# Optimization experiments

Measured on AMD Instinct MI355X. Metric: run time of the kernel, lower is better.

The kernel has to match this reference:

```python
import jax, jax.numpy as jnp
import numpy as np

WINDOW_LENGTH = 128
PAD = WINDOW_LENGTH // 2  # ReflectionPad1d(window_length/2)


def _hanning(w_len, dtype):
    n = jnp.arange(w_len, dtype=jnp.float32)
    w = 0.5 - 0.5 * jnp.cos(2.0 * jnp.pi * n / (w_len - 1))
    return w.astype(dtype)


def setup_inputs() -> dict:
    key = jax.random.key(0)
    seq = jax.random.normal(key, (16, 512, 64), dtype=jnp.float32)
    return {"seq": seq}


def reference(seq):
    B, L, C = seq.shape
    w = _hanning(WINDOW_LENGTH, seq.dtype)  # [W]
    # reflection pad along time, then strided framing via a gather (replaces the cat loop)
    padded = jnp.pad(seq, ((0, 0), (PAD, PAD), (0, 0)), mode="reflect")  # [B, L+2*PAD, C]
    idx = jnp.arange(L)[:, None] + jnp.arange(WINDOW_LENGTH)[None, :]  # [L, W]
    frames = padded[:, idx, :] * w[None, None, :, None]  # [B, L, W, C]
    cube = jnp.fft.rfft(frames, axis=2)  # [B, L, F=W//2+1, C] complex64
    # complex standardization over dims (1, 2): zero-mean, unit second moment per (batch, channel)
    mu = jnp.mean(cube, axis=(1, 2), keepdims=True)
    centered = cube - mu
    std = jnp.sqrt(jnp.mean(jnp.abs(centered) ** 2, axis=(1, 2), keepdims=True))
    normed = centered / std
    return jnp.abs(normed)  # amplitude of the standardized freq cube, [B, L, F, C]
```

## Files before the change

### kernel.cpp

```cpp
#include <hip/hip_runtime.h>
#include <math.h>


#define B_ 16
#define L_ 512
#define C_ 64
#define W_ 128
#define F_ 65
#define LP 640
#define NLF (L_ * F_)

constexpr double kPI = 3.14159265358979323846;

constexpr double csin_(double x) {
  while (x > kPI) x -= 2.0 * kPI;
  while (x < -kPI) x += 2.0 * kPI;
  double t = x, s = x, x2 = x * x;
  for (int i = 1; i <= 24; ++i) {
    t *= -x2 / ((2.0 * i) * (2.0 * i + 1.0));
    s += t;
  }
  return s;
}
constexpr double ccos_(double x) { return csin_(kPI / 2.0 - x); }

constexpr int bitrev6(int n) {
  int r = 0;
  for (int i = 0; i < 6; ++i) r |= ((n >> i) & 1) << (5 - i);
  return r;
}

struct Tables {
  float win[128];
  float walt[128];
  float w2[128];
  float wg[128];
  float twr[32], twi[32];
  float cur[32], cui[32];
  constexpr Tables() : win(), walt(), w2(), wg(), twr(), twi(), cur(), cui() {
    for (int n = 0; n < 128; ++n) {
      const double wd = 0.5 - 0.5 * ccos_(2.0 * kPI * n / 127.0);
      win[n] = (float)wd;
      walt[n] = (n & 1) ? (float)(-wd) : (float)wd;
      w2[n] = (float)(wd * wd);
      if (n == 0) {
        wg[n] = 0.0f;
      } else {
        const double G = csin_(kPI * n / 2.0) * csin_(65.0 * kPI * n / 128.0) /
                         csin_(kPI * n / 128.0);
        wg[n] = (float)(wd * G);
      }
    }
    for (int j = 0; j < 32; ++j) {
      twr[j] = (float)ccos_(2.0 * kPI * j / 64.0);
      twi[j] = (float)(-csin_(2.0 * kPI * j / 64.0));
    }
    for (int k = 0; k < 32; ++k) {
      cur[k] = (float)ccos_(2.0 * kPI * k / 128.0);
      cui[k] = (float)(-csin_(2.0 * kPI * k / 128.0));
    }
  }
};
constexpr Tables TBL{};

__device__ __forceinline__ int refl(int t) {
  const int a = max(t, -t);
  return min(a, 1022 - a);
}

__device__ __forceinline__ float fast_sqrt(float x) {
  float r;
  asm("v_sqrt_f32 %0, %1" : "=v"(r) : "v"(x));
  return r;
}

__global__ void __launch_bounds__(256)
fe_pad_kernel(const float* __restrict__ seq, float* __restrict__ pad) {
  const int idx = blockIdx.x * 256 + threadIdx.x;
  const int c = idx & 63;
  const int row = idx >> 6;
  const int b = row / LP;
  const int t = row - b * LP;
  const int s = refl(t - 64);
  pad[idx] = seq[(b * L_ + s) * C_ + c];
}

__global__ void __launch_bounds__(256)
fe_reduce_kernel(const float* __restrict__ pad, float* __restrict__ acc) {
  const int p = blockIdx.x * 4 + (threadIdx.x >> 6);
  const int b = __builtin_amdgcn_readfirstlane(p >> 9);
  const int l = __builtin_amdgcn_readfirstlane(p & (L_ - 1));
  const int c = threadIdx.x & 63;

  const float* base = pad + ((size_t)(b * LP + l)) * C_ + c;

  float x0 = 0.f, x64 = 0.f, p2 = 0.f, d2 = 0.f;
#pragma unroll
  for (int n = 0; n < 128; ++n) {
    const float v = base[n * C_];
    x0 += TBL.win[n] * v;
    x64 += TBL.walt[n] * v;
    const float wv = TBL.w2[n] * v;
    p2 += wv * v;
    d2 += TBL.wg[n] * v;
  }

  const float sre = 0.5f * (x0 + x64);
  const float sim = -d2;
  const float ssq = 64.0f * p2 + 0.5f * (x0 * x0 + x64 * x64);

  __shared__ float red[3][256];
  const int tid = threadIdx.x;
  red[0][tid] = sre;
  red[1][tid] = sim;
  red[2][tid] = ssq;
  __syncthreads();
  if (tid < 64) {
    const float a0 = red[0][tid] + red[0][tid + 64] + red[0][tid + 128] + red[0][tid + 192];
    const float a1 = red[1][tid] + red[1][tid + 64] + red[1][tid + 128] + red[1][tid + 192];
    const float a2 = red[2][tid] + red[2][tid + 64] + red[2][tid + 128] + red[2][tid + 192];
    const int g = b * C_ + tid;
    unsafeAtomicAdd(&acc[g], a0);
    unsafeAtomicAdd(&acc[1024 + g], a1);
    unsafeAtomicAdd(&acc[2048 + g], a2);
  }
}

__global__ void __launch_bounds__(256, 3)
fe_write_kernel(const float* __restrict__ pad, const float* __restrict__ acc,
                float* __restrict__ out) {
  const int tid = threadIdx.x;
  const int p = blockIdx.x * 4 + (tid >> 6);
  const int b = __builtin_amdgcn_readfirstlane(p >> 9);
  const int l = __builtin_amdgcn_readfirstlane(p & (L_ - 1));
  const int c = tid & 63;

  const int g = b * C_ + c;
  const float invN = 1.0f / (float)NLF;
  const float sr = acc[g] * invN;
  const float si = acc[1024 + g] * invN;
  const float qq = acc[2048 + g] * invN;
  const float var = qq - sr * sr - si * si;
  const float mr = 2.0f * sr;
  const float mi = 2.0f * si;
  const float is = 0.5f * rsqrtf(var);

  const float* base = pad + ((size_t)(b * LP + l)) * C_ + c;

  float zr[64], zi[64];
#pragma unroll
  for (int n = 0; n < 64; ++n) {
    const int m = bitrev6(n);
    zr[n] = TBL.win[2 * m] * base[(2 * m) * C_];
    zi[n] = TBL.win[2 * m + 1] * base[(2 * m + 1) * C_];
  }

#pragma unroll
  for (int s = 0; s < 6; ++s) {
    const int half = 1 << s;
    const int len = half << 1;
#pragma unroll
    for (int j = 0; j < half; ++j) {
      const float wr = TBL.twr[j << (5 - s)];
      const float wi = TBL.twi[j << (5 - s)];
#pragma unroll
      for (int base2 = 0; base2 < 64; base2 += len) {
        const int a = base2 + j;
        const int b2 = a + half;
        const float tr = wr * zr[b2] - wi * zi[b2];
        const float ti = wr * zi[b2] + wi * zr[b2];
        zr[b2] = zr[a] - tr;
        zi[b2] = zi[a] - ti;
        zr[a] += tr;
        zi[a] += ti;
      }
    }
  }

  float* obase = out + (((size_t)(b * L_ + l)) * F_) * C_ + c;
  auto emit = [&](int f, float Xr, float Xi) {
    const float dr = Xr - mr;
    const float di = Xi - mi;
    const float amp = fast_sqrt(__builtin_fmaf(dr, dr, di * di)) * is;
    __builtin_nontemporal_store(amp, &obase[(size_t)f * C_]);
  };

  emit(0, 2.0f * (zr[0] + zi[0]), 0.0f);
  emit(64, 2.0f * (zr[0] - zi[0]), 0.0f);
  emit(32, 2.0f * zr[32], -2.0f * zi[32]);
#pragma unroll
  for (int k = 1; k < 32; ++k) {
    const float cr = TBL.cur[k], ci = TBL.cui[k];
    const float Er = zr[k] + zr[64 - k];
    const float Ei = zi[k] - zi[64 - k];
    const float Or = zi[k] + zi[64 - k];
    const float Oi = zr[64 - k] - zr[k];
    const float wOr = cr * Or - ci * Oi;
    const float wOi = cr * Oi + ci * Or;
    emit(k, Er + wOr, Ei + wOi);
    emit(64 - k, Er - wOr, wOi - Ei);
  }
}

extern "C" void kernel_launch(void* const* d_in, const int* in_sizes, int n_in,
                              void* d_out, int out_size, void* d_ws, size_t ws_size,
                              hipStream_t stream) {
  const float* seq = (const float*)d_in[0];
  float* out = (float*)d_out;
  float* ws = (float*)d_ws;
  float* acc = ws;
  float* pad = ws + 4096;

  hipMemsetAsync(acc, 0, 3072 * sizeof(float), stream);

  fe_pad_kernel<<<(B_ * LP * C_) / 256, 256, 0, stream>>>(seq, pad);
  const int nblocks = (B_ * L_) / 4;
  fe_reduce_kernel<<<nblocks, 256, 0, stream>>>(pad, ws);
  fe_write_kernel<<<nblocks, 256, 0, stream>>>(pad, ws, out);
}
```

Before: 61.57 us.

## Split each 64-point FFT across two lanes with cross-lane shuffle combine

The write kernel now gives each (b,l,c) transform to two lanes. Each lane runs a 32-point FFT on half the even/odd interleaved samples, and partial results are exchanged with __shfl_xor over 32 lanes before the final radix and real-FFT untangling stages. This halves per-thread register arrays and work, which should improve occupancy (launch bounds relaxed) and parallelism. The cost is doubled thread count, shuffles, lane-dependent selects, and channel coverage that is only 32 lanes wide per half-wave, which may affect store coalescing.

Measured after the change: 72.42 us. 17.6% more time.

```diff
diff --git a/kernel.cpp b/kernel.cpp
--- a/kernel.cpp
+++ b/kernel.cpp
@@ -24,9 +24,9 @@
 }
 constexpr double ccos_(double x) { return csin_(kPI / 2.0 - x); }
 
-constexpr int bitrev6(int n) {
+constexpr int bitrev5(int n) {
   int r = 0;
-  for (int i = 0; i < 6; ++i) r |= ((n >> i) & 1) << (5 - i);
+  for (int i = 0; i < 5; ++i) r |= ((n >> i) & 1) << (4 - i);
   return r;
 }
 
@@ -35,9 +35,11 @@
   float walt[128];
   float w2[128];
   float wg[128];
-  float twr[32], twi[32];
-  float cur[32], cui[32];
-  constexpr Tables() : win(), walt(), w2(), wg(), twr(), twi(), cur(), cui() {
+  float t32r[16], t32i[16];
+  float e64r[33], e64i[33];
+  float c128r[33], c128i[33];
+  constexpr Tables()
+      : win(), walt(), w2(), wg(), t32r(), t32i(), e64r(), e64i(), c128r(), c128i() {
     for (int n = 0; n < 128; ++n) {
       const double wd = 0.5 - 0.5 * ccos_(2.0 * kPI * n / 127.0);
       win[n] = (float)wd;
@@ -51,13 +53,15 @@
         wg[n] = (float)(wd * G);
       }
     }
-    for (int j = 0; j < 32; ++j) {
-      twr[j] = (float)ccos_(2.0 * kPI * j / 64.0);
-      twi[j] = (float)(-csin_(2.0 * kPI * j / 64.0));
-    }
-    for (int k = 0; k < 32; ++k) {
-      cur[k] = (float)ccos_(2.0 * kPI * k / 128.0);
-      cui[k] = (float)(-csin_(2.0 * kPI * k / 128.0));
+    for (int r = 0; r < 16; ++r) {
+      t32r[r] = (float)ccos_(2.0 * kPI * r / 32.0);
+      t32i[r] = (float)(-csin_(2.0 * kPI * r / 32.0));
+    }
+    for (int k = 0; k <= 32; ++k) {
+      e64r[k] = (float)ccos_(2.0 * kPI * k / 64.0);
+      e64i[k] = (float)(-csin_(2.0 * kPI * k / 64.0));
+      c128r[k] = (float)ccos_(2.0 * kPI * k / 128.0);
+      c128i[k] = (float)(-csin_(2.0 * kPI * k / 128.0));
     }
   }
 };
@@ -126,14 +130,14 @@
   }
 }
 
-__global__ void __launch_bounds__(256, 3)
+__global__ void __launch_bounds__(256)
 fe_write_kernel(const float* __restrict__ pad, const float* __restrict__ acc,
                 float* __restrict__ out) {
   const int tid = threadIdx.x;
-  const int p = blockIdx.x * 4 + (tid >> 6);
-  const int b = __builtin_amdgcn_readfirstlane(p >> 9);
-  const int l = __builtin_amdgcn_readfirstlane(p & (L_ - 1));
-  const int c = tid & 63;
+  const int lam = (tid >> 5) & 1;
+  const int c = (tid & 31) | (((tid >> 6) & 1) << 5);
+  const int b = __builtin_amdgcn_readfirstlane(blockIdx.x >> 8);
+  const int l = __builtin_amdgcn_readfirstlane(((blockIdx.x & 255) << 1) | (tid >> 7));
 
   const int g = b * C_ + c;
   const float invN = 1.0f / (float)NLF;
@@ -145,60 +149,109 @@
   const float mi = 2.0f * si;
   const float is = 0.5f * rsqrtf(var);
 
-  const float* base = pad + ((size_t)(b * LP + l)) * C_ + c;
-
-  float zr[64], zi[64];
-#pragma unroll
-  for (int n = 0; n < 64; ++n) {
-    const int m = bitrev6(n);
-    zr[n] = TBL.win[2 * m] * base[(2 * m) * C_];
-    zi[n] = TBL.win[2 * m + 1] * base[(2 * m + 1) * C_];
-  }
-
-#pragma unroll
-  for (int s = 0; s < 6; ++s) {
+  const float* base = pad + ((size_t)(b * LP + l)) * C_ + c + (lam << 7);
+
+  float zx[32], zy[32];
+#pragma unroll
+  for (int j = 0; j < 32; ++j) {
+    const int s0 = 4 * bitrev5(j);
+    const float wA = lam ? TBL.win[s0 + 2] : TBL.win[s0];
+    const float wB = lam ? TBL.win[s0 + 3] : TBL.win[s0 + 1];
+    zx[j] = wA * base[s0 * C_];
+    zy[j] = wB * base[s0 * C_ + C_];
+  }
+
+#pragma unroll
+  for (int s = 0; s < 5; ++s) {
     const int half = 1 << s;
     const int len = half << 1;
 #pragma unroll
     for (int j = 0; j < half; ++j) {
-      const float wr = TBL.twr[j << (5 - s)];
-      const float wi = TBL.twi[j << (5 - s)];
-#pragma unroll
-      for (int base2 = 0; base2 < 64; base2 += len) {
+      const float wr = TBL.t32r[j << (4 - s)];
+      const float wi = TBL.t32i[j << (4 - s)];
+#pragma unroll
+      for (int base2 = 0; base2 < 32; base2 += len) {
         const int a = base2 + j;
         const int b2 = a + half;
-        const float tr = wr * zr[b2] - wi * zi[b2];
-        const float ti = wr * zi[b2] + wi * zr[b2];
-        zr[b2] = zr[a] - tr;
-        zi[b2] = zi[a] - ti;
-        zr[a] += tr;
-        zi[a] += ti;
+        const float tr = wr * zx[b2] - wi * zy[b2];
+        const float ti = wr * zy[b2] + wi * zx[b2];
+        zx[b2] = zx[a] - tr;
+        zy[b2] = zy[a] - ti;
+        zx[a] += tr;
+        zy[a] += ti;
       }
     }
   }
 
+  float mx[16], my[16], rx[16], ry[16];
+#pragma unroll
+  for (int j = 0; j < 16; ++j) {
+    const float sx = lam ? zx[2 * j] : zx[2 * j + 1];
+    const float sy = lam ? zy[2 * j] : zy[2 * j + 1];
+    mx[j] = lam ? zx[2 * j + 1] : zx[2 * j];
+    my[j] = lam ? zy[2 * j + 1] : zy[2 * j];
+    rx[j] = __shfl_xor(sx, 32, 64);
+    ry[j] = __shfl_xor(sy, 32, 64);
+  }
+
   float* obase = out + (((size_t)(b * L_ + l)) * F_) * C_ + c;
-  auto emit = [&](int f, float Xr, float Xi) {
+  float* const pK = obase + lam * C_;
+  float* const p64 = obase + (64 - lam) * C_;
+  float* const p3m = obase + (32 - lam) * C_;
+  float* const p3p = obase + (32 + lam) * C_;
+
+  auto emitp = [&](float* p, int off, float Xr, float Xi) {
     const float dr = Xr - mr;
     const float di = Xi - mi;
     const float amp = fast_sqrt(__builtin_fmaf(dr, dr, di * di)) * is;
-    __builtin_nontemporal_store(amp, &obase[(size_t)f * C_]);
+    __builtin_nontemporal_store(amp, p + off);
   };
 
-  emit(0, 2.0f * (zr[0] + zi[0]), 0.0f);
-  emit(64, 2.0f * (zr[0] - zi[0]), 0.0f);
-  emit(32, 2.0f * zr[32], -2.0f * zi[32]);
-#pragma unroll
-  for (int k = 1; k < 32; ++k) {
-    const float cr = TBL.cur[k], ci = TBL.cui[k];
-    const float Er = zr[k] + zr[64 - k];
-    const float Ei = zi[k] - zi[64 - k];
-    const float Or = zi[k] + zi[64 - k];
-    const float Oi = zr[64 - k] - zr[k];
-    const float wOr = cr * Or - ci * Oi;
-    const float wOi = cr * Oi + ci * Or;
-    emit(k, Er + wOr, Ei + wOi);
-    emit(64 - k, Er - wOr, wOi - Ei);
+#pragma unroll
+  for (int t = 0; t <= 8; ++t) {
+    const int i16 = (16 - t) & 15;
+    const float Ekx = lam ? rx[t] : mx[t];
+    const float Eky = lam ? ry[t] : my[t];
+    const float Okx = lam ? mx[t] : rx[t];
+    const float Oky = lam ? my[t] : ry[t];
+    const float Emx = lam ? rx[15 - t] : mx[i16];
+    const float Emy = lam ? ry[15 - t] : my[i16];
+    const float Omx = lam ? mx[15 - t] : rx[i16];
+    const float Omy = lam ? my[15 - t] : ry[i16];
+    const float twkr = lam ? TBL.e64r[2 * t + 1] : TBL.e64r[2 * t];
+    const float twki = lam ? TBL.e64i[2 * t + 1] : TBL.e64i[2 * t];
+    const float twmr = lam ? TBL.e64r[31 - 2 * t] : TBL.e64r[32 - 2 * t];
+    const float twmi = lam ? TBL.e64i[31 - 2 * t] : TBL.e64i[32 - 2 * t];
+    const float ckr = lam ? TBL.c128r[2 * t + 1] : TBL.c128r[2 * t];
+    const float cki = lam ? TBL.c128i[2 * t + 1] : TBL.c128i[2 * t];
+    const float cmr = lam ? TBL.c128r[31 - 2 * t] : TBL.c128r[32 - 2 * t];
+    const float cmi = lam ? TBL.c128i[31 - 2 * t] : TBL.c128i[32 - 2 * t];
+
+    const float akx = twkr * Okx - twki * Oky;
+    const float aky = twkr * Oky + twki * Okx;
+    const float Zkx = Ekx + akx, Zky = Eky + aky;
+    const float Zpx = Ekx - akx, Zpy = Eky - aky;
+    const float bmx = twmr * Omx - twmi * Omy;
+    const float bmy = twmr * Omy + twmi * Omx;
+    const float Zmx = Emx + bmx, Zmy = Emy + bmy;
+    const float Znx = Emx - bmx, Zny = Emy - bmy;
+
+    {
+      const float Er = Zkx + Znx, Ei = Zky - Zny;
+      const float Or2 = Zky + Zny, Oi2 = Znx - Zkx;
+      const float wOr = ckr * Or2 - cki * Oi2;
+      const float wOi = ckr * Oi2 + cki * Or2;
+      emitp(pK, 2 * t * C_, Er + wOr, Ei + wOi);
+      emitp(p64, -2 * t * C_, Er - wOr, wOi - Ei);
+    }
+    {
+      const float Er = Zmx + Zpx, Ei = Zmy - Zpy;
+      const float Or2 = Zmy + Zpy, Oi2 = Zpx - Zmx;
+      const float wOr = cmr * Or2 - cmi * Oi2;
+      const float wOi = cmr * Oi2 + cmi * Or2;
+      emitp(p3m, -2 * t * C_, Er + wOr, Ei + wOi);
+      emitp(p3p, 2 * t * C_, Er - wOr, wOi - Ei);
+    }
   }
 }
 
@@ -214,7 +267,6 @@
   hipMemsetAsync(acc, 0, 3072 * sizeof(float), stream);
 
   fe_pad_kernel<<<(B_ * LP * C_) / 256, 256, 0, stream>>>(seq, pad);
-  const int nblocks = (B_ * L_) / 4;
-  fe_reduce_kernel<<<nblocks, 256, 0, stream>>>(pad, ws);
-  fe_write_kernel<<<nblocks, 256, 0, stream>>>(pad, ws, out);
-}
+  fe_reduce_kernel<<<(B_ * L_) / 4, 256, 0, stream>>>(pad, acc);
+  fe_write_kernel<<<B_ * L_ / 2, 256, 0, stream>>>(pad, acc, out);
+}
```

## Split 64-point FFT into even/odd 32-point halves to cut register pressure

Applied to the files above, without the earlier changes.

The per-thread 64-point complex FFT (real 128-point rFFT) becomes two 32-point FFTs. The first runs on folded sums for the even bins and the second on twiddled differences for the odd bins, each followed by its own real-split postprocessing. This halves the live register arrays, so launch bounds rise from 3 to 4 waves per SIMD. In exchange, the padded input is read from memory twice per thread and there is extra twiddle arithmetic.

New measurement: 77.75 us. 1.26x slower.

```diff
diff --git a/kernel.cpp b/kernel.cpp
--- a/kernel.cpp
+++ b/kernel.cpp
@@ -24,9 +24,9 @@
 }
 constexpr double ccos_(double x) { return csin_(kPI / 2.0 - x); }
 
-constexpr int bitrev6(int n) {
+constexpr int bitrev5(int n) {
   int r = 0;
-  for (int i = 0; i < 6; ++i) r |= ((n >> i) & 1) << (5 - i);
+  for (int i = 0; i < 5; ++i) r |= ((n >> i) & 1) << (4 - i);
   return r;
 }
 
@@ -35,9 +35,11 @@
   float walt[128];
   float w2[128];
   float wg[128];
-  float twr[32], twi[32];
-  float cur[32], cui[32];
-  constexpr Tables() : win(), walt(), w2(), wg(), twr(), twi(), cur(), cui() {
+  float t32r[16], t32i[16];
+  float e64r[32], e64i[32];
+  float c128r[33], c128i[33];
+  constexpr Tables()
+      : win(), walt(), w2(), wg(), t32r(), t32i(), e64r(), e64i(), c128r(), c128i() {
     for (int n = 0; n < 128; ++n) {
       const double wd = 0.5 - 0.5 * ccos_(2.0 * kPI * n / 127.0);
       win[n] = (float)wd;
@@ -51,13 +53,17 @@
         wg[n] = (float)(wd * G);
       }
     }
-    for (int j = 0; j < 32; ++j) {
-      twr[j] = (float)ccos_(2.0 * kPI * j / 64.0);
-      twi[j] = (float)(-csin_(2.0 * kPI * j / 64.0));
-    }
-    for (int k = 0; k < 32; ++k) {
-      cur[k] = (float)ccos_(2.0 * kPI * k / 128.0);
-      cui[k] = (float)(-csin_(2.0 * kPI * k / 128.0));
+    for (int r = 0; r < 16; ++r) {
+      t32r[r] = (float)ccos_(2.0 * kPI * r / 32.0);
+      t32i[r] = (float)(-csin_(2.0 * kPI * r / 32.0));
+    }
+    for (int p = 0; p < 32; ++p) {
+      e64r[p] = (float)ccos_(2.0 * kPI * p / 64.0);
+      e64i[p] = (float)(-csin_(2.0 * kPI * p / 64.0));
+    }
+    for (int k = 0; k <= 32; ++k) {
+      c128r[k] = (float)ccos_(2.0 * kPI * k / 128.0);
+      c128i[k] = (float)(-csin_(2.0 * kPI * k / 128.0));
     }
   }
 };
@@ -126,7 +132,31 @@
   }
 }
 
-__global__ void __launch_bounds__(256, 3)
+__device__ __forceinline__ void fft32(float* __restrict__ ur, float* __restrict__ ui) {
+#pragma unroll
+  for (int s = 0; s < 5; ++s) {
+    const int half = 1 << s;
+    const int len = half << 1;
+#pragma unroll
+    for (int j = 0; j < half; ++j) {
+      const float wr = TBL.t32r[j << (4 - s)];
+      const float wi = TBL.t32i[j << (4 - s)];
+#pragma unroll
+      for (int base2 = 0; base2 < 32; base2 += len) {
+        const int a = base2 + j;
+        const int b2 = a + half;
+        const float tr = wr * ur[b2] - wi * ui[b2];
+        const float ti = wr * ui[b2] + wi * ur[b2];
+        ur[b2] = ur[a] - tr;
+        ui[b2] = ui[a] - ti;
+        ur[a] += tr;
+        ui[a] += ti;
+      }
+    }
+  }
+}
+
+__global__ void __launch_bounds__(256, 4)
 fe_write_kernel(const float* __restrict__ pad, const float* __restrict__ acc,
                 float* __restrict__ out) {
   const int tid = threadIdx.x;
@@ -146,38 +176,8 @@
   const float is = 0.5f * rsqrtf(var);
 
   const float* base = pad + ((size_t)(b * LP + l)) * C_ + c;
-
-  float zr[64], zi[64];
-#pragma unroll
-  for (int n = 0; n < 64; ++n) {
-    const int m = bitrev6(n);
-    zr[n] = TBL.win[2 * m] * base[(2 * m) * C_];
-    zi[n] = TBL.win[2 * m + 1] * base[(2 * m + 1) * C_];
-  }
-
-#pragma unroll
-  for (int s = 0; s < 6; ++s) {
-    const int half = 1 << s;
-    const int len = half << 1;
-#pragma unroll
-    for (int j = 0; j < half; ++j) {
-      const float wr = TBL.twr[j << (5 - s)];
-      const float wi = TBL.twi[j << (5 - s)];
-#pragma unroll
-      for (int base2 = 0; base2 < 64; base2 += len) {
-        const int a = base2 + j;
-        const int b2 = a + half;
-        const float tr = wr * zr[b2] - wi * zi[b2];
-        const float ti = wr * zi[b2] + wi * zr[b2];
-        zr[b2] = zr[a] - tr;
-        zi[b2] = zi[a] - ti;
-        zr[a] += tr;
-        zi[a] += ti;
-      }
-    }
-  }
-
   float* obase = out + (((size_t)(b * L_ + l)) * F_) * C_ + c;
+
   auto emit = [&](int f, float Xr, float Xi) {
     const float dr = Xr - mr;
     const float di = Xi - mi;
@@ -185,20 +185,63 @@
     __builtin_nontemporal_store(amp, &obase[(size_t)f * C_]);
   };
 
-  emit(0, 2.0f * (zr[0] + zi[0]), 0.0f);
-  emit(64, 2.0f * (zr[0] - zi[0]), 0.0f);
-  emit(32, 2.0f * zr[32], -2.0f * zi[32]);
-#pragma unroll
-  for (int k = 1; k < 32; ++k) {
-    const float cr = TBL.cur[k], ci = TBL.cui[k];
-    const float Er = zr[k] + zr[64 - k];
-    const float Ei = zi[k] - zi[64 - k];
-    const float Or = zi[k] + zi[64 - k];
-    const float Oi = zr[64 - k] - zr[k];
+  float ur[32], ui[32];
+
+#pragma unroll
+  for (int j = 0; j < 32; ++j) {
+    const int q = bitrev5(j);
+    const float a0 = TBL.win[2 * q] * base[(2 * q) * C_];
+    const float a1 = TBL.win[2 * q + 1] * base[(2 * q + 1) * C_];
+    const float b0 = TBL.win[2 * q + 64] * base[(2 * q + 64) * C_];
+    const float b1 = TBL.win[2 * q + 65] * base[(2 * q + 65) * C_];
+    ur[j] = a0 + b0;
+    ui[j] = a1 + b1;
+  }
+  fft32(ur, ui);
+
+  emit(0, 2.0f * (ur[0] + ui[0]), 0.0f);
+  emit(64, 2.0f * (ur[0] - ui[0]), 0.0f);
+  emit(32, 2.0f * ur[16], -2.0f * ui[16]);
+#pragma unroll
+  for (int t = 1; t < 16; ++t) {
+    const int u2 = 32 - t;
+    const float cr = TBL.c128r[2 * t], ci = TBL.c128i[2 * t];
+    const float Er = ur[t] + ur[u2];
+    const float Ei = ui[t] - ui[u2];
+    const float Or = ui[t] + ui[u2];
+    const float Oi = ur[u2] - ur[t];
     const float wOr = cr * Or - ci * Oi;
     const float wOi = cr * Oi + ci * Or;
-    emit(k, Er + wOr, Ei + wOi);
-    emit(64 - k, Er - wOr, wOi - Ei);
+    emit(2 * t, Er + wOr, Ei + wOi);
+    emit(64 - 2 * t, Er - wOr, wOi - Ei);
+  }
+
+#pragma unroll
+  for (int j = 0; j < 32; ++j) {
+    const int q = bitrev5(j);
+    const float a0 = TBL.win[2 * q] * base[(2 * q) * C_];
+    const float a1 = TBL.win[2 * q + 1] * base[(2 * q + 1) * C_];
+    const float b0 = TBL.win[2 * q + 64] * base[(2 * q + 64) * C_];
+    const float b1 = TBL.win[2 * q + 65] * base[(2 * q + 65) * C_];
+    const float vr = a0 - b0;
+    const float vi = a1 - b1;
+    ur[j] = TBL.e64r[q] * vr - TBL.e64i[q] * vi;
+    ui[j] = TBL.e64r[q] * vi + TBL.e64i[q] * vr;
+  }
+  fft32(ur, ui);
+
+#pragma unroll
+  for (int t = 0; t < 16; ++t) {
+    const int u2 = 31 - t;
+    const float cr = TBL.c128r[2 * t + 1], ci = TBL.c128i[2 * t + 1];
+    const float Er = ur[t] + ur[u2];
+    const float Ei = ui[t] - ui[u2];
+    const float Or = ui[t] + ui[u2];
+    const float Oi = ur[u2] - ur[t];
+    const float wOr = cr * Or - ci * Oi;
+    const float wOi = cr * Oi + ci * Or;
+    emit(2 * t + 1, Er + wOr, Ei + wOi);
+    emit(63 - 2 * t, Er - wOr, wOi - Ei);
   }
 }
 
@@ -214,7 +257,6 @@
   hipMemsetAsync(acc, 0, 3072 * sizeof(float), stream);
 
   fe_pad_kernel<<<(B_ * LP * C_) / 256, 256, 0, stream>>>(seq, pad);
-  const int nblocks = (B_ * L_) / 4;
-  fe_reduce_kernel<<<nblocks, 256, 0, stream>>>(pad, ws);
-  fe_write_kernel<<<nblocks, 256, 0, stream>>>(pad, ws, out);
-}
+  fe_reduce_kernel<<<(B_ * L_) / 4, 256, 0, stream>>>(pad, acc);
+  fe_write_kernel<<<(B_ * L_) / 4, 256, 0, stream>>>(pad, acc, out);
+}
```

## Split each frame's 64-point FFT across four waves with LDS transpose

Applied to the files above, without the earlier changes.

Before, one thread ran the whole 64-point complex FFT for a frame and channel in registers (128 floats). Now each block handles a single frame: its four waves each run a 16-point sub-FFT, exchange results through a 64x64 float2 LDS buffer, and finish the last two radix stages plus the real-FFT post-processing in a distributed way. This cuts per-thread register pressure and raises occupancy and parallelism (4x more blocks). The cost is three block barriers, LDS traffic, and partner reads from LDS when producing outputs.

Result: slower. 74.91 us (+21.7%).

```diff
diff --git a/kernel.cpp b/kernel.cpp
--- a/kernel.cpp
+++ b/kernel.cpp
@@ -24,9 +24,9 @@
 }
 constexpr double ccos_(double x) { return csin_(kPI / 2.0 - x); }
 
-constexpr int bitrev6(int n) {
+constexpr int bitrev4(int n) {
   int r = 0;
-  for (int i = 0; i < 6; ++i) r |= ((n >> i) & 1) << (5 - i);
+  for (int i = 0; i < 4; ++i) r |= ((n >> i) & 1) << (3 - i);
   return r;
 }
 
@@ -35,9 +35,10 @@
   float walt[128];
   float w2[128];
   float wg[128];
-  float twr[32], twi[32];
-  float cur[32], cui[32];
-  constexpr Tables() : win(), walt(), w2(), wg(), twr(), twi(), cur(), cui() {
+  float t64r[32], t64i[32];
+  float c128r[64], c128i[64];
+  constexpr Tables()
+      : win(), walt(), w2(), wg(), t64r(), t64i(), c128r(), c128i() {
     for (int n = 0; n < 128; ++n) {
       const double wd = 0.5 - 0.5 * ccos_(2.0 * kPI * n / 127.0);
       win[n] = (float)wd;
@@ -52,12 +53,12 @@
       }
     }
     for (int j = 0; j < 32; ++j) {
-      twr[j] = (float)ccos_(2.0 * kPI * j / 64.0);
-      twi[j] = (float)(-csin_(2.0 * kPI * j / 64.0));
-    }
-    for (int k = 0; k < 32; ++k) {
-      cur[k] = (float)ccos_(2.0 * kPI * k / 128.0);
-      cui[k] = (float)(-csin_(2.0 * kPI * k / 128.0));
+      t64r[j] = (float)ccos_(2.0 * kPI * j / 64.0);
+      t64i[j] = (float)(-csin_(2.0 * kPI * j / 64.0));
+    }
+    for (int k = 0; k < 64; ++k) {
+      c128r[k] = (float)ccos_(2.0 * kPI * k / 128.0);
+      c128i[k] = (float)(-csin_(2.0 * kPI * k / 128.0));
     }
   }
 };
@@ -126,14 +127,16 @@
   }
 }
 
-__global__ void __launch_bounds__(256, 3)
+__global__ void __launch_bounds__(256)
 fe_write_kernel(const float* __restrict__ pad, const float* __restrict__ acc,
                 float* __restrict__ out) {
+  __shared__ float2 lds[64][64];
+
   const int tid = threadIdx.x;
-  const int p = blockIdx.x * 4 + (tid >> 6);
-  const int b = __builtin_amdgcn_readfirstlane(p >> 9);
-  const int l = __builtin_amdgcn_readfirstlane(p & (L_ - 1));
+  const int n4 = __builtin_amdgcn_readfirstlane(tid >> 6);
   const int c = tid & 63;
+  const int frame = __builtin_amdgcn_readfirstlane(blockIdx.x);
+  const int b = frame >> 9;
 
   const int g = b * C_ + c;
   const float invN = 1.0f / (float)NLF;
@@ -145,61 +148,121 @@
   const float mi = 2.0f * si;
   const float is = 0.5f * rsqrtf(var);
 
+  const int l = frame & 511;
   const float* base = pad + ((size_t)(b * LP + l)) * C_ + c;
-
-  float zr[64], zi[64];
-#pragma unroll
-  for (int n = 0; n < 64; ++n) {
-    const int m = bitrev6(n);
-    zr[n] = TBL.win[2 * m] * base[(2 * m) * C_];
-    zi[n] = TBL.win[2 * m + 1] * base[(2 * m + 1) * C_];
-  }
-
-#pragma unroll
-  for (int s = 0; s < 6; ++s) {
+  float* obase = out + ((size_t)frame * F_) * C_ + c;
+
+  const int brn4 = ((n4 & 1) << 1) | (n4 >> 1);
+
+  float zr[16], zi[16];
+#pragma unroll
+  for (int i = 0; i < 16; ++i) {
+    const int row = 8 * bitrev4(i) + 2 * brn4;
+    zr[i] = TBL.win[row] * base[row * C_];
+    zi[i] = TBL.win[row + 1] * base[(row + 1) * C_];
+  }
+
+#pragma unroll
+  for (int s = 0; s < 4; ++s) {
     const int half = 1 << s;
     const int len = half << 1;
 #pragma unroll
     for (int j = 0; j < half; ++j) {
-      const float wr = TBL.twr[j << (5 - s)];
-      const float wi = TBL.twi[j << (5 - s)];
-#pragma unroll
-      for (int base2 = 0; base2 < 64; base2 += len) {
-        const int a = base2 + j;
-        const int b2 = a + half;
-        const float tr = wr * zr[b2] - wi * zi[b2];
-        const float ti = wr * zi[b2] + wi * zr[b2];
-        zr[b2] = zr[a] - tr;
-        zi[b2] = zi[a] - ti;
+      const float wr = TBL.t64r[j << (5 - s)];
+      const float wi = TBL.t64i[j << (5 - s)];
+#pragma unroll
+      for (int b2 = 0; b2 < 16; b2 += len) {
+        const int a = b2 + j;
+        const int bb = a + half;
+        const float tr = wr * zr[bb] - wi * zi[bb];
+        const float ti = wr * zi[bb] + wi * zr[bb];
+        zr[bb] = zr[a] - tr;
+        zi[bb] = zi[a] - ti;
         zr[a] += tr;
         zi[a] += ti;
       }
     }
   }
 
-  float* obase = out + (((size_t)(b * L_ + l)) * F_) * C_ + c;
-  auto emit = [&](int f, float Xr, float Xi) {
+#pragma unroll
+  for (int i = 0; i < 16; ++i)
+    lds[16 * n4 + i][c] = make_float2(zr[i], zi[i]);
+  __syncthreads();
+#pragma unroll
+  for (int u = 0; u < 4; ++u)
+#pragma unroll
+    for (int t = 0; t < 4; ++t) {
+      const float2 v = lds[4 * n4 + u + 16 * t][c];
+      zr[4 * u + t] = v.x;
+      zi[4 * u + t] = v.y;
+    }
+  __syncthreads();
+
+#pragma unroll
+  for (int u = 0; u < 4; ++u) {
+    {
+      const int jj = (4 * n4 + u) << 1;
+      const float wr = TBL.t64r[jj], wi = TBL.t64i[jj];
+#pragma unroll
+      for (int t0 = 0; t0 < 4; t0 += 2) {
+        const int a = 4 * u + t0, bb = a + 1;
+        const float tr = wr * zr[bb] - wi * zi[bb];
+        const float ti = wr * zi[bb] + wi * zr[bb];
+        zr[bb] = zr[a] - tr;
+        zi[bb] = zi[a] - ti;
+        zr[a] += tr;
+        zi[a] += ti;
+      }
+    }
+#pragma unroll
+    for (int t0 = 0; t0 < 2; ++t0) {
+      const int jj = 4 * n4 + u + 16 * t0;
+      const float wr = TBL.t64r[jj], wi = TBL.t64i[jj];
+      const int a = 4 * u + t0, bb = a + 2;
+      const float tr = wr * zr[bb] - wi * zi[bb];
+      const float ti = wr * zi[bb] + wi * zr[bb];
+      zr[bb] = zr[a] - tr;
+      zi[bb] = zi[a] - ti;
+      zr[a] += tr;
+      zi[a] += ti;
+    }
+  }
+
+#pragma unroll
+  for (int u = 0; u < 4; ++u)
+#pragma unroll
+    for (int t = 0; t < 4; ++t)
+      lds[4 * n4 + u + 16 * t][c] = make_float2(zr[4 * u + t], zi[4 * u + t]);
+  __syncthreads();
+
+  auto emit = [&](int foff, float Xr, float Xi) {
     const float dr = Xr - mr;
     const float di = Xi - mi;
     const float amp = fast_sqrt(__builtin_fmaf(dr, dr, di * di)) * is;
-    __builtin_nontemporal_store(amp, &obase[(size_t)f * C_]);
+    __builtin_nontemporal_store(amp, obase + foff);
   };
 
-  emit(0, 2.0f * (zr[0] + zi[0]), 0.0f);
-  emit(64, 2.0f * (zr[0] - zi[0]), 0.0f);
-  emit(32, 2.0f * zr[32], -2.0f * zi[32]);
-#pragma unroll
-  for (int k = 1; k < 32; ++k) {
-    const float cr = TBL.cur[k], ci = TBL.cui[k];
-    const float Er = zr[k] + zr[64 - k];
-    const float Ei = zi[k] - zi[64 - k];
-    const float Or = zi[k] + zi[64 - k];
-    const float Oi = zr[64 - k] - zr[k];
-    const float wOr = cr * Or - ci * Oi;
-    const float wOi = cr * Oi + ci * Or;
-    emit(k, Er + wOr, Ei + wOi);
-    emit(64 - k, Er - wOr, wOi - Ei);
-  }
+#pragma unroll
+  for (int u = 0; u < 4; ++u)
+#pragma unroll
+    for (int t = 0; t < 4; ++t) {
+      const int idx = 4 * u + t;
+      const int P = 4 * n4 + u + 16 * t;
+      if (n4 == 0 && u == 0 && t == 0) {
+        emit(0, 2.0f * (zr[0] + zi[0]), 0.0f);
+        emit(64 * C_, 2.0f * (zr[0] - zi[0]), 0.0f);
+      } else {
+        const float2 o = lds[64 - P][c];
+        const float Er = zr[idx] + o.x;
+        const float Ei = zi[idx] - o.y;
+        const float Or = zi[idx] + o.y;
+        const float Oi = o.x - zr[idx];
+        const float cr = TBL.c128r[P], ci = TBL.c128i[P];
+        const float wOr = cr * Or - ci * Oi;
+        const float wOi = cr * Oi + ci * Or;
+        emit(P * C_, Er + wOr, Ei + wOi);
+      }
+    }
 }
 
 extern "C" void kernel_launch(void* const* d_in, const int* in_sizes, int n_in,
@@ -214,7 +277,6 @@
   hipMemsetAsync(acc, 0, 3072 * sizeof(float), stream);
 
   fe_pad_kernel<<<(B_ * LP * C_) / 256, 256, 0, stream>>>(seq, pad);
-  const int nblocks = (B_ * L_) / 4;
-  fe_reduce_kernel<<<nblocks, 256, 0, stream>>>(pad, ws);
-  fe_write_kernel<<<nblocks, 256, 0, stream>>>(pad, ws, out);
-}
+  fe_reduce_kernel<<<(B_ * L_) / 4, 256, 0, stream>>>(pad, acc);
+  fe_write_kernel<<<B_ * L_, 256, 0, stream>>>(pad, acc, out);
+}
```
